# Performance work log

Hardware: AMD Instinct MI355X
Metric: run time of the kernel (lower is better)

The kernel has to match this reference:

```python
import jax, jax.numpy as jnp
import numpy as np
from jax import lax

B, C_IN, N, C_OUT, K = 16, 128, 2048, 256, 20
EPS = 1e-5


def setup_inputs() -> dict:
    key = jax.random.key(0)
    k1, k2 = jax.random.split(key)
    x = jax.random.normal(k1, (B, C_IN, N), dtype=jnp.float32)
    W = jax.random.normal(k2, (C_OUT, 2 * C_IN), dtype=jnp.float32) * (1.0 / np.sqrt(2 * C_IN))
    gamma = jnp.ones((C_OUT,), dtype=jnp.float32)
    beta = jnp.zeros((C_OUT,), dtype=jnp.float32)
    return {"x": x, "W": W, "gamma": gamma, "beta": beta, "k": K}


def _knn_inds(x, k):
    # squared pairwise distance: (B, N, N); computed with no grad (stop_gradient)
    xs = lax.stop_gradient(x)
    inner = jnp.einsum('bcn,bcm->bnm', xs, xs)
    sq = jnp.sum(xs * xs, axis=1)  # (B, N)
    pd = sq[:, :, None] - 2.0 * inner + sq[:, None, :]
    _, inds = lax.top_k(-pd, k)  # smallest distances -> (B, N, k)
    return inds


def reference(x, W, gamma, beta, k):
    knn = _knn_inds(x, k)                                   # (B, N, k) int
    # gather neighbours: neigh[b,c,n,j] = x[b,c,knn[b,n,j]]
    neigh = jax.vmap(lambda xb, kb: xb[:, kb])(x, knn)      # (B, C, N, k)
    central = jnp.broadcast_to(x[:, :, :, None], neigh.shape)
    edge = jnp.concatenate([central, neigh - central], axis=1)  # (B, 2C, N, k)
    # 1x1 conv (bias-free) as GEMM
    y = jnp.einsum('oc,bcnk->bonk', W, edge)                # (B, C_out, N, k)
    # BatchNorm2d (training-mode batch stats) + affine
    mean = jnp.mean(y, axis=(0, 2, 3), keepdims=True)
    var = jnp.var(y, axis=(0, 2, 3), keepdims=True)
    y = (y - mean) * lax.rsqrt(var + EPS)
    y = y * gamma[None, :, None, None] + beta[None, :, None, None]
    y = jax.nn.relu(y)
    return jnp.max(y, axis=3)                               # (B, C_out, N)
```

## Files before the change

### kernel.cpp

```cpp
#include <hip/hip_runtime.h>

#define B_   16
#define CIN  128
#define NPT  2048
#define COUT 256
#define KNN  20
#define KEEP 16
#define CAND 64
#define SIFT 32
#define EPS  1e-5f
#define DBIAS 256.0f

#define SQ_OFF   0ull
#define IDX_OFF  131072ull
#define UT_OFF   2752512ull
#define VT_OFF   36306944ull
#define GS_OFF   69861376ull
#define ST_OFF   69865472ull
#define AMAX_OFF 69871616ull
#define AMIN_OFF 103426048ull
#define WS_NEED_FUSED 136980480ull
#define XT_OFF   UT_OFF
#define XHT_OFF  VT_OFF

typedef _Float16 f16x8 __attribute__((ext_vector_type(8)));
typedef float    f32x4 __attribute__((ext_vector_type(4)));
typedef float    f32x2 __attribute__((ext_vector_type(2)));

__global__ __launch_bounds__(256) void prep_kernel(const float* __restrict__ x,
                                                   float* __restrict__ xT,
                                                   _Float16* __restrict__ xhT,
                                                   float* __restrict__ sqh) {
    __shared__ float Ls[128 * 68];
    __shared__ float ps[4 * 64];
    const int b = blockIdx.y, n0 = blockIdx.x * 64, t = threadIdx.x;
    const float* xb = x + (size_t)b * CIN * NPT;
    #pragma unroll
    for (int e = 0; e < 8; ++e) {
        int f = e * 256 + t;
        int c = f >> 4, n4 = (f & 15) << 2;
        *(float4*)&Ls[c * 68 + n4] = *(const float4*)&xb[(size_t)c * NPT + n0 + n4];
    }
    __syncthreads();
    {
        int nl = t & 63, part = t >> 6;
        float acc = 0.f;
        #pragma unroll
        for (int j = 0; j < 32; ++j) {
            float vh = (float)(_Float16)Ls[(part * 32 + j) * 68 + nl];
            acc += vh * vh;
        }
        ps[part * 64 + nl] = acc;
    }
    #pragma unroll
    for (int e = 0; e < 2; ++e) {
        int u = e * 256 + t;
        int nl = u >> 3, ck = (u & 7) << 4;
        float vv[16];
        #pragma unroll
        for (int j = 0; j < 16; ++j) vv[j] = Ls[(ck + j) * 68 + nl];
        size_t row = (size_t)b * NPT + n0 + nl;
        #pragma unroll
        for (int j = 0; j < 4; ++j) {
            float4 w = {vv[4 * j], vv[4 * j + 1], vv[4 * j + 2], vv[4 * j + 3]};
            *(float4*)&xT[row * CIN + ck + 4 * j] = w;
        }
        f16x8 h0, h1;
        #pragma unroll
        for (int j = 0; j < 8; ++j) { h0[j] = (_Float16)vv[j]; h1[j] = (_Float16)vv[8 + j]; }
        *(f16x8*)&xhT[row * CIN + ck] = h0;
        *(f16x8*)&xhT[row * CIN + ck + 8] = h1;
    }
    __syncthreads();
    if (t < 64) sqh[b * NPT + n0 + t] = ps[t] + ps[64 + t] + ps[128 + t] + ps[192 + t];
}

__global__ void wconv_kernel(const float* __restrict__ W,
                             _Float16* __restrict__ Wu,
                             _Float16* __restrict__ Wv) {
    int gid = blockIdx.x * 256 + threadIdx.x;
    int o = gid >> 7, c = gid & 127;
    float w1 = W[o * 256 + c], w2 = W[o * 256 + 128 + c];
    Wu[gid] = (_Float16)(w1 - w2);
    Wv[gid] = (_Float16)w2;
}

__device__ __forceinline__ void stage_pts(const _Float16* __restrict__ xhb,
                                          _Float16* buf, int base_n, int t) {
    const int l15 = t & 15, ks = t >> 6;
    const int quad = (t >> 4) & 3;
    const int c = ks * 32 + quad * 8;
    #pragma unroll
    for (int e = 0; e < 4; ++e) {
        const int n = base_n + e * 16 + l15;
        const _Float16* src = xhb + (size_t)n * CIN + c;
        _Float16* dst = buf + (size_t)(e * 256 + (t & 192)) * 8;
        __builtin_amdgcn_global_load_lds(
            (const __attribute__((address_space(1))) void*)src,
            (__attribute__((address_space(3))) void*)dst, 16, 0, 0);
    }
}

__device__ __forceinline__ void stage_tile16(const _Float16* __restrict__ srcl,
                                             _Float16* dsthalf) {
    #pragma unroll
    for (int e = 0; e < 4; ++e) {
        __builtin_amdgcn_global_load_lds(
            (const __attribute__((address_space(1))) void*)(srcl + e * 32),
            (__attribute__((address_space(3))) void*)(dsthalf + (size_t)e * 512),
            16, 0, 0);
    }
}

__global__ __launch_bounds__(256, 2) void knn_kernel(const _Float16* __restrict__ xhT,
                                                     const float* __restrict__ xT,
                                                     const float* __restrict__ sqh,
                                                     int* __restrict__ knn_out) {
    __shared__ char smraw[59392];
    _Float16* bufA = (_Float16*)smraw;
    float*    sqm  = (float*)(smraw + 18432);

    const int b  = blockIdx.y;
    const int q0 = blockIdx.x * 64;
    const int t  = threadIdx.x;
    const int lane = t & 63, wv = t >> 6;
    const int l15 = lane & 15, quad = lane >> 4;
    const _Float16* xhb = xhT + (size_t)b * NPT * CIN;

    #pragma unroll
    for (int e = 0; e < 8; ++e)
        sqm[e * 256 + t] = sqh[b * NPT + e * 256 + t] + DBIAS;

    stage_pts(xhb, bufA, q0, t);
    __syncthreads();

    f16x8 af[4][4];
    #pragma unroll
    for (int qh = 0; qh < 4; ++qh)
        #pragma unroll
        for (int ks = 0; ks < 4; ++ks)
            af[qh][ks] = *(const f16x8*)(bufA + (size_t)((qh * 4 + ks) * 64 + lane) * 8);
    __syncthreads();

    _Float16* wbuf = (_Float16*)(smraw + 26624 + wv * 8192);
    float*    DtW  = (float*)(smraw + wv * 4608);
    const _Float16* srcl = xhb + (size_t)(wv * 16 + l15) * CIN + quad * 8;

    stage_tile16(srcl, wbuf);

    float bd[KEEP];
    #pragma unroll
    for (int i = 0; i < KEEP; ++i) bd[i] = 3.0e38f;

    #pragma unroll 1
    for (int ss = 0; ss < 32; ++ss) {
        const int mb = ss * 64 + wv * 16;
        asm volatile("s_waitcnt vmcnt(0)" ::: "memory");
        __builtin_amdgcn_sched_barrier(0);
        const _Float16* cur = wbuf + (ss & 1) * 2048;
        f16x8 bf[4];
        #pragma unroll
        for (int ks = 0; ks < 4; ++ks)
            bf[ks] = *(const f16x8*)(cur + ks * 512 + quad * 128 + l15 * 8);
        float sm_ = sqm[mb + l15];
        asm volatile("s_waitcnt lgkmcnt(0)" ::: "memory");
        __builtin_amdgcn_sched_barrier(0);
        if (ss < 31)
            stage_tile16(srcl + (size_t)(ss + 1) * 64 * CIN,
                         wbuf + ((ss + 1) & 1) * 2048);
        __builtin_amdgcn_sched_barrier(0);
        f32x4 acc[4];
        #pragma unroll
        for (int qh = 0; qh < 4; ++qh) acc[qh] = (f32x4){0.f, 0.f, 0.f, 0.f};
        #pragma unroll
        for (int ks = 0; ks < 4; ++ks)
            #pragma unroll
            for (int qh = 0; qh < 4; ++qh)
                acc[qh] = __builtin_amdgcn_mfma_f32_16x16x32_f16(af[qh][ks], bf[ks], acc[qh], 0, 0, 0);
        const unsigned om = (unsigned)(mb + l15);
        #pragma unroll
        for (int qh = 0; qh < 4; ++qh) {
            #pragma unroll
            for (int rg = 0; rg < 4; ++rg) {
                int q = qh * 16 + quad * 4 + rg;
                float d = sm_ - 2.f * acc[qh][rg];
                DtW[q * 18 + l15] = __uint_as_float((__float_as_uint(d) & 0xFFFFF800u) | om);
            }
        }
        float nk[16];
        {
            const float* myrow = DtW + lane * 18;
            #pragma unroll
            for (int p = 0; p < 8; ++p) {
                f32x2 v = *(const f32x2*)(myrow + 2 * p);
                nk[2 * p] = v[0]; nk[2 * p + 1] = v[1];
            }
        }
        #pragma unroll
        for (int kk = 2; kk <= 16; kk <<= 1) {
            #pragma unroll
            for (int j = kk >> 1; j > 0; j >>= 1) {
                #pragma unroll
                for (int i = 0; i < 16; ++i) {
                    int p = i ^ j;
                    if (p > i) {
                        float a = nk[i], c = nk[p];
                        float lo = fminf(a, c), hi = fmaxf(a, c);
                        if ((i & kk) == 0) { nk[i] = lo; nk[p] = hi; }
                        else               { nk[i] = hi; nk[p] = lo; }
                    }
                }
            }
        }
        #pragma unroll
        for (int i = 0; i < 16; ++i) bd[i] = fminf(bd[i], nk[15 - i]);
        #pragma unroll
        for (int j = 8; j > 0; j >>= 1) {
            #pragma unroll
            for (int i = 0; i < 16; ++i) {
                int p = i ^ j;
                if (p > i) {
                    float a = bd[i], c = bd[p];
                    bd[i] = fminf(a, c);
                    bd[p] = fmaxf(a, c);
                }
            }
        }
    }

    __syncthreads();

    float*  Keys = (float*)smraw;
    int*    Surv = (int*)(smraw + 16640);
    double* ddL  = (double*)(smraw + 25088);
    #pragma unroll
    for (int i = 0; i < KEEP; ++i)
        Keys[lane * 65 + wv * KEEP + i] = bd[i];
    __syncthreads();
    {
        int cnt[KEEP];
        #pragma unroll
        for (int i = 0; i < KEEP; ++i) cnt[i] = 0;
        #pragma unroll 4
        for (int j = 0; j < CAND; ++j) {
            float kj = Keys[lane * 65 + j];
            #pragma unroll
            for (int i = 0; i < KEEP; ++i)
                cnt[i] += (kj < bd[i]) ? 1 : 0;
        }
        __syncthreads();
        #pragma unroll
        for (int i = 0; i < KEEP; ++i)
            if (cnt[i] < SIFT)
                Surv[lane * 33 + cnt[i]] = (int)(__float_as_uint(bd[i]) & 0x7FFu);
    }
    __syncthreads();

    int ms[8];
    #pragma unroll
    for (int k = 0; k < 8; ++k) ms[k] = Surv[lane * 33 + wv * 8 + k] & 2047;
    double dd8[8];
    #pragma unroll
    for (int k = 0; k < 8; ++k) dd8[k] = 0.0;
    const float* xTb = xT + (size_t)b * NPT * CIN;
    const float* qrow = xTb + (size_t)(q0 + lane) * CIN;
    #pragma unroll 1
    for (int ch = 0; ch < 8; ++ch) {
        double qd[16];
        #pragma unroll
        for (int j = 0; j < 4; ++j) {
            float4 qv = *(const float4*)&qrow[ch * 16 + 4 * j];
            qd[4 * j] = (double)qv.x; qd[4 * j + 1] = (double)qv.y;
            qd[4 * j + 2] = (double)qv.z; qd[4 * j + 3] = (double)qv.w;
        }
        #pragma unroll
        for (int k = 0; k < 8; ++k) {
            const float* mrow = xTb + (size_t)ms[k] * CIN + ch * 16;
            float4 ma = *(const float4*)&mrow[0];
            float4 mb2 = *(const float4*)&mrow[4];
            float4 mc = *(const float4*)&mrow[8];
            float4 md = *(const float4*)&mrow[12];
            double ss = dd8[k], d0;
            d0 = qd[0]  - (double)ma.x;  ss = fma(d0, d0, ss);
            d0 = qd[1]  - (double)ma.y;  ss = fma(d0, d0, ss);
            d0 = qd[2]  - (double)ma.z;  ss = fma(d0, d0, ss);
            d0 = qd[3]  - (double)ma.w;  ss = fma(d0, d0, ss);
            d0 = qd[4]  - (double)mb2.x; ss = fma(d0, d0, ss);
            d0 = qd[5]  - (double)mb2.y; ss = fma(d0, d0, ss);
            d0 = qd[6]  - (double)mb2.z; ss = fma(d0, d0, ss);
            d0 = qd[7]  - (double)mb2.w; ss = fma(d0, d0, ss);
            d0 = qd[8]  - (double)mc.x;  ss = fma(d0, d0, ss);
            d0 = qd[9]  - (double)mc.y;  ss = fma(d0, d0, ss);
            d0 = qd[10] - (double)mc.z;  ss = fma(d0, d0, ss);
            d0 = qd[11] - (double)mc.w;  ss = fma(d0, d0, ss);
            d0 = qd[12] - (double)md.x;  ss = fma(d0, d0, ss);
            d0 = qd[13] - (double)md.y;  ss = fma(d0, d0, ss);
            d0 = qd[14] - (double)md.z;  ss = fma(d0, d0, ss);
            d0 = qd[15] - (double)md.w;  ss = fma(d0, d0, ss);
            dd8[k] = ss;
        }
    }

    #pragma unroll
    for (int k = 0; k < 8; ++k) ddL[lane * 33 + wv * 8 + k] = dd8[k];
    __syncthreads();
    int* dst = knn_out + ((size_t)b * NPT + q0 + lane) * KNN;
    #pragma unroll
    for (int k = 0; k < 8; ++k) {
        int c = 0;
        #pragma unroll 4
        for (int j = 0; j < SIFT; ++j)
            c += (ddL[lane * 33 + j] < dd8[k]) ? 1 : 0;
        if (c < KNN) dst[c] = ms[k];
    }
}

__global__ __launch_bounds__(256) void uv_gemm_h(const _Float16* __restrict__ xhT,
                                                 const _Float16* __restrict__ Wu,
                                                 const _Float16* __restrict__ Wv,
                                                 float* __restrict__ uT,
                                                 float* __restrict__ vT) {
    __shared__ _Float16 Bx[8192];
    const int b = blockIdx.y, n0 = blockIdx.x * 64, t = threadIdx.x;
    const int lane = t & 63, w = t >> 6, l15 = lane & 15, quad = lane >> 4;
    stage_pts(xhT + (size_t)b * NPT * CIN, Bx, n0, t);
    __syncthreads();
    f16x8 bf[4];
    #pragma unroll
    for (int ks = 0; ks < 4; ++ks)
        bf[ks] = *(const f16x8*)(Bx + (size_t)((w * 4 + ks) * 64 + lane) * 8);
    const int n = n0 + w * 16 + l15;
    #pragma unroll 1
    for (int ot = 0; ot < 16; ++ot) {
        const _Float16* wu = Wu + (size_t)(ot * 16 + l15) * 128 + quad * 8;
        const _Float16* wv2 = Wv + (size_t)(ot * 16 + l15) * 128 + quad * 8;
        f32x4 au = (f32x4){0.f, 0.f, 0.f, 0.f};
        f32x4 av = (f32x4){0.f, 0.f, 0.f, 0.f};
        #pragma unroll
        for (int ks = 0; ks < 4; ++ks) {
            f16x8 a_u = *(const f16x8*)(wu + ks * 32);
            f16x8 a_v = *(const f16x8*)(wv2 + ks * 32);
            au = __builtin_amdgcn_mfma_f32_16x16x32_f16(a_u, bf[ks], au, 0, 0, 0);
            av = __builtin_amdgcn_mfma_f32_16x16x32_f16(a_v, bf[ks], av, 0, 0, 0);
        }
        size_t base = ((size_t)b * NPT + n) * COUT + ot * 16 + quad * 4;
        *(f32x4*)&uT[base] = au;
        *(f32x4*)&vT[base] = av;
    }
}

__global__ __launch_bounds__(256) void uv_gemm(const float* __restrict__ x,
                                               const float* __restrict__ W,
                                               float* __restrict__ uT,
                                               float* __restrict__ vT) {
    __shared__ float Ax[32 * 64];
    __shared__ float Bu[32 * 68];
    __shared__ float Bv[32 * 68];
    const int b  = blockIdx.z;
    const int n0 = blockIdx.x * 64;
    const int o0 = blockIdx.y * 64;
    const int t  = threadIdx.x;
    const int tx = t & 15, ty = t >> 4;
    const float* xb = x + (size_t)b * CIN * NPT;
    float au[4][4], av_[4][4];
    #pragma unroll
    for (int i = 0; i < 4; ++i)
        #pragma unroll
        for (int j = 0; j < 4; ++j) { au[i][j] = 0.f; av_[i][j] = 0.f; }
    #pragma unroll 1
    for (int kc = 0; kc < 4; ++kc) {
        const int c0 = kc * 32;
        __syncthreads();
        #pragma unroll
        for (int e = 0; e < 2; ++e) {
            int f = e * 256 + t;
            int cz = f >> 4, ni = (f & 15) << 2;
            *(float4*)&Ax[(cz << 6) + ni] = *(const float4*)&xb[(size_t)(c0 + cz) * NPT + n0 + ni];
        }
        #pragma unroll
        for (int e = 0; e < 8; ++e) {
            int ii = e * 256 + t;
            int cz = ii & 31, oj = ii >> 5;
            float w1 = W[(size_t)(o0 + oj) * 256 + c0 + cz];
            float w2 = W[(size_t)(o0 + oj) * 256 + 128 + c0 + cz];
            Bu[cz * 68 + oj] = w1 - w2;
            Bv[cz * 68 + oj] = w2;
        }
        __syncthreads();
        #pragma unroll 8
        for (int cz = 0; cz < 32; ++cz) {
            const float4 a4 = *(const float4*)&Ax[(cz << 6) + (tx << 2)];
            float bu0 = Bu[cz * 68 + (ty << 2) + 0], bv0 = Bv[cz * 68 + (ty << 2) + 0];
            float bu1 = Bu[cz * 68 + (ty << 2) + 1], bv1 = Bv[cz * 68 + (ty << 2) + 1];
            float bu2 = Bu[cz * 68 + (ty << 2) + 2], bv2 = Bv[cz * 68 + (ty << 2) + 2];
            float bu3 = Bu[cz * 68 + (ty << 2) + 3], bv3 = Bv[cz * 68 + (ty << 2) + 3];
            au[0][0] += a4.x * bu0; au[0][1] += a4.x * bu1; au[0][2] += a4.x * bu2; au[0][3] += a4.x * bu3;
            au[1][0] += a4.y * bu0; au[1][1] += a4.y * bu1; au[1][2] += a4.y * bu2; au[1][3] += a4.y * bu3;
            au[2][0] += a4.z * bu0; au[2][1] += a4.z * bu1; au[2][2] += a4.z * bu2; au[2][3] += a4.z * bu3;
            au[3][0] += a4.w * bu0; au[3][1] += a4.w * bu1; au[3][2] += a4.w * bu2; au[3][3] += a4.w * bu3;
            av_[0][0] += a4.x * bv0; av_[0][1] += a4.x * bv1; av_[0][2] += a4.x * bv2; av_[0][3] += a4.x * bv3;
            av_[1][0] += a4.y * bv0; av_[1][1] += a4.y * bv1; av_[1][2] += a4.y * bv2; av_[1][3] += a4.y * bv3;
            av_[2][0] += a4.z * bv0; av_[2][1] += a4.z * bv1; av_[2][2] += a4.z * bv2; av_[2][3] += a4.z * bv3;
            av_[3][0] += a4.w * bv0; av_[3][1] += a4.w * bv1; av_[3][2] += a4.w * bv2; av_[3][3] += a4.w * bv3;
        }
    }
    #pragma unroll
    for (int i = 0; i < 4; ++i) {
        int n = n0 + (tx << 2) + i;
        size_t base = ((size_t)b * NPT + n) * COUT + o0 + (ty << 2);
        float4 u4 = {au[i][0], au[i][1], au[i][2], au[i][3]};
        float4 v4 = {av_[i][0], av_[i][1], av_[i][2], av_[i][3]};
        *(float4*)&uT[base] = u4;
        *(float4*)&vT[base] = v4;
    }
}

__global__ __launch_bounds__(256) void gather_stats(const float* __restrict__ uT,
                                                    const float* __restrict__ vT,
                                                    const int* __restrict__ knn_in,
                                                    double* __restrict__ gsum,
                                                    float* __restrict__ aMax,
                                                    float* __restrict__ aMin) {
    __shared__ int sidx[16 * KNN];
    const int b  = blockIdx.y;
    const int n0 = blockIdx.x * 64 + blockIdx.z * 16;
    const int o  = threadIdx.x;
    for (int e = o; e < 16 * KNN; e += 256)
        sidx[e] = knn_in[((size_t)b * NPT + n0) * KNN + e];
    __syncthreads();
    const float* ub = uT + ((size_t)b * NPT + n0) * COUT + o;
    const float* vb = vT + (size_t)b * NPT * COUT + o;
    float* amx = aMax + ((size_t)b * NPT + n0) * COUT + o;
    float* amn = aMin + ((size_t)b * NPT + n0) * COUT + o;
    double s1 = 0.0, s2 = 0.0;
    #pragma unroll 1
    for (int s = 0; s < 16; ++s) {
        float u = ub[(size_t)s * COUT];
        float vmax = -3e38f, vmin = 3e38f, vsum = 0.f, vsq = 0.f;
        #pragma unroll
        for (int j = 0; j < KNN; ++j) {
            float v = vb[(size_t)sidx[s * KNN + j] * COUT];
            vmax = fmaxf(vmax, v);
            vmin = fminf(vmin, v);
            vsum += v;
            vsq = fmaf(v, v, vsq);
        }
        s1 += 20.0 * (double)u + (double)vsum;
        s2 += 20.0 * (double)u * (double)u + 2.0 * (double)u * (double)vsum + (double)vsq;
        amx[(size_t)s * COUT] = vmax;
        amn[(size_t)s * COUT] = vmin;
    }
    atomicAdd(&gsum[o], s1);
    atomicAdd(&gsum[COUT + o], s2);
}

__global__ __launch_bounds__(256) void stats_kernel(const float* __restrict__ uT,
                                                    const float* __restrict__ vT,
                                                    const int* __restrict__ knn_in,
                                                    double* __restrict__ gsum) {
    __shared__ int sidx[64 * KNN];
    const int b  = blockIdx.y;
    const int n0 = blockIdx.x * 64;
    const int o  = threadIdx.x;
    for (int e = o; e < 64 * KNN; e += 256)
        sidx[e] = knn_in[((size_t)b * NPT + n0) * KNN + e];
    __syncthreads();
    const float* ub = uT + ((size_t)b * NPT + n0) * COUT + o;
    const float* vb = vT + (size_t)b * NPT * COUT + o;
    double s1 = 0.0, s2 = 0.0;
    #pragma unroll 1
    for (int s = 0; s < 64; ++s) {
        float u = ub[(size_t)s * COUT];
        #pragma unroll
        for (int j = 0; j < KNN; ++j) {
            float y = u + vb[(size_t)sidx[s * KNN + j] * COUT];
            s1 += (double)y;
            s2 = fma((double)y, (double)y, s2);
        }
    }
    atomicAdd(&gsum[o], s1);
    atomicAdd(&gsum[COUT + o], s2);
}

__global__ void finalize_kernel(const double* __restrict__ gsum,
                                const float* __restrict__ gamma,
                                const float* __restrict__ beta,
                                float* __restrict__ st) {
    const int o = threadIdx.x;
    const double M = (double)B_ * NPT * KNN;
    double mean = gsum[o] / M;
    double var  = gsum[COUT + o] / M - mean * mean;
    float inv = 1.0f / sqrtf((float)var + EPS);
    float s = gamma[o] * inv;
    st[o] = s;
    st[COUT + o] = beta[o] - (float)mean * s;
}

__global__ __launch_bounds__(256, 2) void out2_kernel(const float* __restrict__ uT,
                                                      const float* __restrict__ aMax,
                                                      const float* __restrict__ aMin,
                                                      const float* __restrict__ st,
                                                      float* __restrict__ out) {
    __shared__ float zt[256 * 68];
    const int b  = blockIdx.y;
    const int n0 = blockIdx.x * 64;
    const int o  = threadIdx.x;
    const float s  = st[o];
    const float tt = st[COUT + o];
    const float* ub  = uT   + ((size_t)b * NPT + n0) * COUT + o;
    const float* amx = aMax + ((size_t)b * NPT + n0) * COUT + o;
    const float* amn = aMin + ((size_t)b * NPT + n0) * COUT + o;
    #pragma unroll 2
    for (int si = 0; si < 64; ++si) {
        float u = ub[(size_t)si * COUT];
        float y1 = u + amx[(size_t)si * COUT];
        float y2 = u + amn[(size_t)si * COUT];
        float z1 = fmaxf(s * y1 + tt, 0.f);
        float z2 = fmaxf(s * y2 + tt, 0.f);
        zt[o * 68 + si] = fmaxf(z1, z2);
    }
    __syncthreads();
    float* dst = out + ((size_t)b * COUT + o) * NPT + n0;
    #pragma unroll
    for (int i = 0; i < 16; ++i)
        *(float4*)&dst[i * 4] = *(const float4*)&zt[o * 68 + i * 4];
}

__global__ __launch_bounds__(256, 2) void out_kernel(const float* __restrict__ uT,
                                                     const float* __restrict__ vT,
                                                     const int* __restrict__ knn_in,
                                                     const float* __restrict__ st,
                                                     float* __restrict__ out) {
    __shared__ int sidx[64 * KNN];
    __shared__ float zt[256 * 68];
    const int b  = blockIdx.y;
    const int n0 = blockIdx.x * 64;
    const int o  = threadIdx.x;
    for (int e = o; e < 64 * KNN; e += 256)
        sidx[e] = knn_in[((size_t)b * NPT + n0) * KNN + e];
    __syncthreads();
    const float s  = st[o];
    const float tt = st[COUT + o];
    const float* ub = uT + ((size_t)b * NPT + n0) * COUT + o;
    const float* vb = vT + (size_t)b * NPT * COUT + o;
    #pragma unroll 1
    for (int si = 0; si < 64; ++si) {
        float u = ub[(size_t)si * COUT];
        float ymax = -3e38f, ymin = 3e38f;
        #pragma unroll
        for (int j = 0; j < KNN; ++j) {
            float y = u + vb[(size_t)sidx[si * KNN + j] * COUT];
            ymax = fmaxf(ymax, y);
            ymin = fminf(ymin, y);
        }
        float z1 = fmaxf(s * ymax + tt, 0.f);
        float z2 = fmaxf(s * ymin + tt, 0.f);
        zt[o * 68 + si] = fmaxf(z1, z2);
    }
    __syncthreads();
    float* dst = out + ((size_t)b * COUT + o) * NPT + n0;
    #pragma unroll
    for (int i = 0; i < 16; ++i)
        *(float4*)&dst[i * 4] = *(const float4*)&zt[o * 68 + i * 4];
}

extern "C" void kernel_launch(void* const* d_in, const int* in_sizes, int n_in,
                              void* d_out, int out_size, void* d_ws, size_t ws_size,
                              hipStream_t stream) {
    const float* x     = (const float*)d_in[0];
    const float* W     = (const float*)d_in[1];
    const float* gamma = (const float*)d_in[2];
    const float* beta  = (const float*)d_in[3];
    float* out = (float*)d_out;
    char* ws = (char*)d_ws;
    float*     sqh  = (float*)(ws + SQ_OFF);
    int*       idx  = (int*)(ws + IDX_OFF);
    float*     uT   = (float*)(ws + UT_OFF);
    float*     vT   = (float*)(ws + VT_OFF);
    double*    gsum = (double*)(ws + GS_OFF);
    float*     st   = (float*)(ws + ST_OFF);
    float*     aMax = (float*)(ws + AMAX_OFF);
    float*     aMin = (float*)(ws + AMIN_OFF);
    const bool fused = (ws_size >= WS_NEED_FUSED);

    hipMemsetAsync(gsum, 0, 2 * COUT * sizeof(double), stream);
    if (fused) {
        float*    xT  = (float*)(ws + AMAX_OFF);
        _Float16* xhT = (_Float16*)(ws + AMAX_OFF + 16777216ull);
        _Float16* Wu  = (_Float16*)(ws + AMAX_OFF + 25165824ull);
        _Float16* Wv  = (_Float16*)(ws + AMAX_OFF + 25231360ull);
        prep_kernel<<<dim3(32, 16), 256, 0, stream>>>(x, xT, xhT, sqh);
        wconv_kernel<<<128, 256, 0, stream>>>(W, Wu, Wv);
        knn_kernel<<<dim3(32, 16), 256, 0, stream>>>(xhT, xT, sqh, idx);
        uv_gemm_h<<<dim3(32, 16), 256, 0, stream>>>(xhT, Wu, Wv, uT, vT);
        gather_stats<<<dim3(32, 16, 4), 256, 0, stream>>>(uT, vT, idx, gsum, aMax, aMin);
        finalize_kernel<<<1, 256, 0, stream>>>(gsum, gamma, beta, st);
        out2_kernel<<<dim3(32, 16), 256, 0, stream>>>(uT, aMax, aMin, st, out);
    } else {
        float*    xT  = (float*)(ws + XT_OFF);
        _Float16* xhT = (_Float16*)(ws + XHT_OFF);
        prep_kernel<<<dim3(32, 16), 256, 0, stream>>>(x, xT, xhT, sqh);
        knn_kernel<<<dim3(32, 16), 256, 0, stream>>>(xhT, xT, sqh, idx);
        uv_gemm<<<dim3(32, 4, 16), 256, 0, stream>>>(x, W, uT, vT);
        stats_kernel<<<dim3(32, 16), 256, 0, stream>>>(uT, vT, idx, gsum);
        finalize_kernel<<<1, 256, 0, stream>>>(gsum, gamma, beta, st);
        out_kernel<<<dim3(32, 16), 256, 0, stream>>>(uT, vT, idx, st, out);
    }
}
```

Before: 352.2 us.

## Split kNN wave work into 32-query by 16-candidate tiles

Each wave in the kNN kernel now covers 32 queries against a 16-candidate tile over 64 steps, instead of all 64 queries over 32 steps. Each query's 64-candidate pool is spread across four sub-lists. Per step a lane sorts 8 new distances instead of 16 and merges them into the upper half of its kept list. This roughly halves the A-fragment registers and the LDS scratch per wave, and the next tile's prefetch is now issued before the current tile's reads. In exchange there are twice as many loop iterations, each running a full 16-wide merge, so total sorting work and loop overhead may grow.

```diff
diff --git a/kernel.cpp b/kernel.cpp
--- a/kernel.cpp
+++ b/kernel.cpp
@@ -116,15 +116,17 @@
                                                      const float* __restrict__ xT,
                                                      const float* __restrict__ sqh,
                                                      int* __restrict__ knn_out) {
-    __shared__ char smraw[59392];
+    __shared__ char smraw[57344];
     _Float16* bufA = (_Float16*)smraw;
-    float*    sqm  = (float*)(smraw + 18432);
+    float*    sqm  = (float*)(smraw + 16384);
 
     const int b  = blockIdx.y;
     const int q0 = blockIdx.x * 64;
     const int t  = threadIdx.x;
     const int lane = t & 63, wv = t >> 6;
     const int l15 = lane & 15, quad = lane >> 4;
+    const int qh2 = wv & 1;
+    const int mh  = wv >> 1;
     const _Float16* xhb = xhT + (size_t)b * NPT * CIN;
 
     #pragma unroll
@@ -134,74 +136,74 @@
     stage_pts(xhb, bufA, q0, t);
     __syncthreads();
 
-    f16x8 af[4][4];
-    #pragma unroll
-    for (int qh = 0; qh < 4; ++qh)
-        #pragma unroll
-        for (int ks = 0; ks < 4; ++ks)
-            af[qh][ks] = *(const f16x8*)(bufA + (size_t)((qh * 4 + ks) * 64 + lane) * 8);
-    __syncthreads();
-
-    _Float16* wbuf = (_Float16*)(smraw + 26624 + wv * 8192);
-    float*    DtW  = (float*)(smraw + wv * 4608);
-    const _Float16* srcl = xhb + (size_t)(wv * 16 + l15) * CIN + quad * 8;
-
+    f16x8 af0[4], af1[4];
+    #pragma unroll
+    for (int ks = 0; ks < 4; ++ks) {
+        af0[ks] = *(const f16x8*)(bufA + (size_t)((qh2 * 2) * 2048 + ks * 512 + lane * 8));
+        af1[ks] = *(const f16x8*)(bufA + (size_t)((qh2 * 2 + 1) * 2048 + ks * 512 + lane * 8));
+    }
+
+    _Float16* wbuf = (_Float16*)(smraw + 24576 + wv * 8192);
+    const _Float16* srcl = xhb + (size_t)(mh * 16 + l15) * CIN + quad * 8;
     stage_tile16(srcl, wbuf);
 
+    __syncthreads();
+    float* DtW = (float*)(smraw + wv * 2304);
+
     float bd[KEEP];
     #pragma unroll
     for (int i = 0; i < KEEP; ++i) bd[i] = 3.0e38f;
 
     #pragma unroll 1
-    for (int ss = 0; ss < 32; ++ss) {
-        const int mb = ss * 64 + wv * 16;
+    for (int ss = 0; ss < 64; ++ss) {
+        const int mb = (ss * 2 + mh) << 4;
         asm volatile("s_waitcnt vmcnt(0)" ::: "memory");
         __builtin_amdgcn_sched_barrier(0);
-        const _Float16* cur = wbuf + (ss & 1) * 2048;
-        f16x8 bf[4];
-        #pragma unroll
-        for (int ks = 0; ks < 4; ++ks)
-            bf[ks] = *(const f16x8*)(cur + ks * 512 + quad * 128 + l15 * 8);
-        float sm_ = sqm[mb + l15];
-        asm volatile("s_waitcnt lgkmcnt(0)" ::: "memory");
-        __builtin_amdgcn_sched_barrier(0);
-        if (ss < 31)
-            stage_tile16(srcl + (size_t)(ss + 1) * 64 * CIN,
+        if (ss < 63)
+            stage_tile16(srcl + (size_t)(ss + 1) * 32 * CIN,
                          wbuf + ((ss + 1) & 1) * 2048);
         __builtin_amdgcn_sched_barrier(0);
-        f32x4 acc[4];
-        #pragma unroll
-        for (int qh = 0; qh < 4; ++qh) acc[qh] = (f32x4){0.f, 0.f, 0.f, 0.f};
-        #pragma unroll
-        for (int ks = 0; ks < 4; ++ks)
+        const _Float16* cur = wbuf + (ss & 1) * 2048;
+        f16x8 bf0 = *(const f16x8*)(cur + 0 * 512 + lane * 8);
+        f16x8 bf1 = *(const f16x8*)(cur + 1 * 512 + lane * 8);
+        f16x8 bf2 = *(const f16x8*)(cur + 2 * 512 + lane * 8);
+        f16x8 bf3 = *(const f16x8*)(cur + 3 * 512 + lane * 8);
+        float sm_ = sqm[mb + l15];
+        f32x4 acc0 = (f32x4){0.f, 0.f, 0.f, 0.f};
+        f32x4 acc1 = (f32x4){0.f, 0.f, 0.f, 0.f};
+        acc0 = __builtin_amdgcn_mfma_f32_16x16x32_f16(af0[0], bf0, acc0, 0, 0, 0);
+        acc1 = __builtin_amdgcn_mfma_f32_16x16x32_f16(af1[0], bf0, acc1, 0, 0, 0);
+        acc0 = __builtin_amdgcn_mfma_f32_16x16x32_f16(af0[1], bf1, acc0, 0, 0, 0);
+        acc1 = __builtin_amdgcn_mfma_f32_16x16x32_f16(af1[1], bf1, acc1, 0, 0, 0);
+        acc0 = __builtin_amdgcn_mfma_f32_16x16x32_f16(af0[2], bf2, acc0, 0, 0, 0);
+        acc1 = __builtin_amdgcn_mfma_f32_16x16x32_f16(af1[2], bf2, acc1, 0, 0, 0);
+        acc0 = __builtin_amdgcn_mfma_f32_16x16x32_f16(af0[3], bf3, acc0, 0, 0, 0);
+        acc1 = __builtin_amdgcn_mfma_f32_16x16x32_f16(af1[3], bf3, acc1, 0, 0, 0);
+        const unsigned om = (unsigned)(mb + l15);
+        #pragma unroll
+        for (int rg = 0; rg < 4; ++rg) {
+            float d0 = sm_ - 2.f * acc0[rg];
+            DtW[(quad * 4 + rg) * 18 + l15] =
+                __uint_as_float((__float_as_uint(d0) & 0xFFFFF800u) | om);
+            float d1 = sm_ - 2.f * acc1[rg];
+            DtW[(16 + quad * 4 + rg) * 18 + l15] =
+                __uint_as_float((__float_as_uint(d1) & 0xFFFFF800u) | om);
+        }
+        float nk[8];
+        {
+            const float* myrow = DtW + (lane & 31) * 18 + (lane >> 5) * 8;
             #pragma unroll
-            for (int qh = 0; qh < 4; ++qh)
-                acc[qh] = __builtin_amdgcn_mfma_f32_16x16x32_f16(af[qh][ks], bf[ks], acc[qh], 0, 0, 0);
-        const unsigned om = (unsigned)(mb + l15);
-        #pragma unroll
-        for (int qh = 0; qh < 4; ++qh) {
-            #pragma unroll
-            for (int rg = 0; rg < 4; ++rg) {
-                int q = qh * 16 + quad * 4 + rg;
-                float d = sm_ - 2.f * acc[qh][rg];
-                DtW[q * 18 + l15] = __uint_as_float((__float_as_uint(d) & 0xFFFFF800u) | om);
-            }
-        }
-        float nk[16];
-        {
-            const float* myrow = DtW + lane * 18;
-            #pragma unroll
-            for (int p = 0; p < 8; ++p) {
+            for (int p = 0; p < 4; ++p) {
                 f32x2 v = *(const f32x2*)(myrow + 2 * p);
                 nk[2 * p] = v[0]; nk[2 * p + 1] = v[1];
             }
         }
         #pragma unroll
-        for (int kk = 2; kk <= 16; kk <<= 1) {
+        for (int kk = 2; kk <= 8; kk <<= 1) {
             #pragma unroll
             for (int j = kk >> 1; j > 0; j >>= 1) {
                 #pragma unroll
-                for (int i = 0; i < 16; ++i) {
+                for (int i = 0; i < 8; ++i) {
                     int p = i ^ j;
                     if (p > i) {
                         float a = nk[i], c = nk[p];
@@ -213,7 +215,7 @@
             }
         }
         #pragma unroll
-        for (int i = 0; i < 16; ++i) bd[i] = fminf(bd[i], nk[15 - i]);
+        for (int i = 0; i < 8; ++i) bd[8 + i] = fminf(bd[8 + i], nk[7 - i]);
         #pragma unroll
         for (int j = 8; j > 0; j >>= 1) {
             #pragma unroll
@@ -233,9 +235,11 @@
     float*  Keys = (float*)smraw;
     int*    Surv = (int*)(smraw + 16640);
     double* ddL  = (double*)(smraw + 25088);
+    const int q   = qh2 * 32 + (lane & 31);
+    const int sub = mh * 2 + (lane >> 5);
     #pragma unroll
     for (int i = 0; i < KEEP; ++i)
-        Keys[lane * 65 + wv * KEEP + i] = bd[i];
+        Keys[q * 65 + sub * KEEP + i] = bd[i];
     __syncthreads();
     {
         int cnt[KEEP];
@@ -243,7 +247,7 @@
         for (int i = 0; i < KEEP; ++i) cnt[i] = 0;
         #pragma unroll 4
         for (int j = 0; j < CAND; ++j) {
-            float kj = Keys[lane * 65 + j];
+            float kj = Keys[q * 65 + j];
             #pragma unroll
             for (int i = 0; i < KEEP; ++i)
                 cnt[i] += (kj < bd[i]) ? 1 : 0;
@@ -252,18 +256,18 @@
         #pragma unroll
         for (int i = 0; i < KEEP; ++i)
             if (cnt[i] < SIFT)
-                Surv[lane * 33 + cnt[i]] = (int)(__float_as_uint(bd[i]) & 0x7FFu);
+                Surv[q * 33 + cnt[i]] = (int)(__float_as_uint(bd[i]) & 0x7FFu);
     }
     __syncthreads();
 
     int ms[8];
     #pragma unroll
-    for (int k = 0; k < 8; ++k) ms[k] = Surv[lane * 33 + wv * 8 + k] & 2047;
+    for (int k = 0; k < 8; ++k) ms[k] = Surv[q * 33 + sub * 8 + k] & 2047;
     double dd8[8];
     #pragma unroll
     for (int k = 0; k < 8; ++k) dd8[k] = 0.0;
     const float* xTb = xT + (size_t)b * NPT * CIN;
-    const float* qrow = xTb + (size_t)(q0 + lane) * CIN;
+    const float* qrow = xTb + (size_t)(q0 + q) * CIN;
     #pragma unroll 1
     for (int ch = 0; ch < 8; ++ch) {
         double qd[16];
@@ -302,15 +306,15 @@
     }
 
     #pragma unroll
-    for (int k = 0; k < 8; ++k) ddL[lane * 33 + wv * 8 + k] = dd8[k];
-    __syncthreads();
-    int* dst = knn_out + ((size_t)b * NPT + q0 + lane) * KNN;
+    for (int k = 0; k < 8; ++k) ddL[q * 33 + sub * 8 + k] = dd8[k];
+    __syncthreads();
+    int* dst = knn_out + ((size_t)b * NPT + q0 + q) * KNN;
     #pragma unroll
     for (int k = 0; k < 8; ++k) {
         int c = 0;
         #pragma unroll 4
         for (int j = 0; j < SIFT; ++j)
-            c += (ddL[lane * 33 + j] < dd8[k]) ? 1 : 0;
+            c += (ddL[q * 33 + j] < dd8[k]) ? 1 : 0;
         if (c < KNN) dst[c] = ms[k];
     }
 }
```

Measured after the change: 369.2 us. 4.8% more time.

## Split kNN exact refinement into separate high-occupancy refine kernel

Applied to the files above, without the earlier changes.

The fp16 MFMA kNN kernel now stops after its candidate merge and writes 32 surviving candidate indices per query to workspace. A new refine_kernel, launched over 16-query blocks, recomputes the exact fp64 distances for those candidates and ranks them to produce the final 20 neighbours. The goal is to move the serial fp64 refinement out of the low-occupancy MFMA kernel and spread it across many more blocks. The cost is an extra launch and a workspace round trip for the survivor list. The old fused version is kept as knn_kernel_fb for the smaller-workspace fallback path.

```diff
diff --git a/kernel.cpp b/kernel.cpp
--- a/kernel.cpp
+++ b/kernel.cpp
@@ -113,9 +113,8 @@
 }
 
 __global__ __launch_bounds__(256, 2) void knn_kernel(const _Float16* __restrict__ xhT,
-                                                     const float* __restrict__ xT,
                                                      const float* __restrict__ sqh,
-                                                     int* __restrict__ knn_out) {
+                                                     int* __restrict__ surv_out) {
     __shared__ char smraw[59392];
     _Float16* bufA = (_Float16*)smraw;
     float*    sqm  = (float*)(smraw + 18432);
@@ -161,7 +160,219 @@
         f16x8 bf[4];
         #pragma unroll
         for (int ks = 0; ks < 4; ++ks)
-            bf[ks] = *(const f16x8*)(cur + ks * 512 + quad * 128 + l15 * 8);
+            bf[ks] = *(const f16x8*)(cur + ks * 512 + lane * 8);
+        float sm_ = sqm[mb + l15];
+        asm volatile("s_waitcnt lgkmcnt(0)" ::: "memory");
+        __builtin_amdgcn_sched_barrier(0);
+        if (ss < 31)
+            stage_tile16(srcl + (size_t)(ss + 1) * 64 * CIN,
+                         wbuf + ((ss + 1) & 1) * 2048);
+        __builtin_amdgcn_sched_barrier(0);
+        f32x4 acc[4];
+        #pragma unroll
+        for (int qh = 0; qh < 4; ++qh) acc[qh] = (f32x4){0.f, 0.f, 0.f, 0.f};
+        #pragma unroll
+        for (int ks = 0; ks < 4; ++ks)
+            #pragma unroll
+            for (int qh = 0; qh < 4; ++qh)
+                acc[qh] = __builtin_amdgcn_mfma_f32_16x16x32_f16(af[qh][ks], bf[ks], acc[qh], 0, 0, 0);
+        const unsigned om = (unsigned)(mb + l15);
+        #pragma unroll
+        for (int qh = 0; qh < 4; ++qh) {
+            #pragma unroll
+            for (int rg = 0; rg < 4; ++rg) {
+                int q = qh * 16 + quad * 4 + rg;
+                float d = sm_ - 2.f * acc[qh][rg];
+                DtW[q * 18 + l15] = __uint_as_float((__float_as_uint(d) & 0xFFFFF800u) | om);
+            }
+        }
+        float nk[16];
+        {
+            const float* myrow = DtW + lane * 18;
+            #pragma unroll
+            for (int p = 0; p < 8; ++p) {
+                f32x2 v = *(const f32x2*)(myrow + 2 * p);
+                nk[2 * p] = v[0]; nk[2 * p + 1] = v[1];
+            }
+        }
+        #pragma unroll
+        for (int kk = 2; kk <= 16; kk <<= 1) {
+            #pragma unroll
+            for (int j = kk >> 1; j > 0; j >>= 1) {
+                #pragma unroll
+                for (int i = 0; i < 16; ++i) {
+                    int p = i ^ j;
+                    if (p > i) {
+                        float a = nk[i], c = nk[p];
+                        float lo = fminf(a, c), hi = fmaxf(a, c);
+                        if ((i & kk) == 0) { nk[i] = lo; nk[p] = hi; }
+                        else               { nk[i] = hi; nk[p] = lo; }
+                    }
+                }
+            }
+        }
+        #pragma unroll
+        for (int i = 0; i < 16; ++i) bd[i] = fminf(bd[i], nk[15 - i]);
+        #pragma unroll
+        for (int j = 8; j > 0; j >>= 1) {
+            #pragma unroll
+            for (int i = 0; i < 16; ++i) {
+                int p = i ^ j;
+                if (p > i) {
+                    float a = bd[i], c = bd[p];
+                    bd[i] = fminf(a, c);
+                    bd[p] = fmaxf(a, c);
+                }
+            }
+        }
+    }
+
+    __syncthreads();
+
+    float* Keys = (float*)smraw;
+    #pragma unroll
+    for (int i = 0; i < KEEP; ++i)
+        Keys[lane * 65 + wv * KEEP + i] = bd[i];
+    __syncthreads();
+    {
+        int cnt[KEEP];
+        #pragma unroll
+        for (int i = 0; i < KEEP; ++i) cnt[i] = 0;
+        #pragma unroll 4
+        for (int j = 0; j < CAND; ++j) {
+            float kj = Keys[lane * 65 + j];
+            #pragma unroll
+            for (int i = 0; i < KEEP; ++i)
+                cnt[i] += (kj < bd[i]) ? 1 : 0;
+        }
+        int* dst = surv_out + ((size_t)b * NPT + q0 + lane) * SIFT;
+        #pragma unroll
+        for (int i = 0; i < KEEP; ++i)
+            if (cnt[i] < SIFT)
+                dst[cnt[i]] = (int)(__float_as_uint(bd[i]) & 0x7FFu);
+    }
+}
+
+__global__ __launch_bounds__(256, 4) void refine_kernel(const float* __restrict__ xT,
+                                                        const int* __restrict__ surv,
+                                                        int* __restrict__ knn_out) {
+    __shared__ float  Qs[16 * 128];
+    __shared__ int    sidx[16 * 32];
+    __shared__ double ddL[16 * 32];
+    const int b = blockIdx.y, q0 = blockIdx.x * 16, t = threadIdx.x;
+    const float* xTb = xT + (size_t)b * NPT * CIN;
+    #pragma unroll
+    for (int e = 0; e < 2; ++e)
+        sidx[e * 256 + t] = surv[((size_t)b * NPT + q0) * SIFT + e * 256 + t];
+    #pragma unroll
+    for (int e = 0; e < 2; ++e) {
+        int f = e * 256 + t;
+        int row = f >> 5, c4 = (f & 31) << 2;
+        *(float4*)&Qs[row * 128 + c4] = *(const float4*)&xTb[(size_t)(q0 + row) * CIN + c4];
+    }
+    __syncthreads();
+    const int g = t >> 3, j = t & 7;
+    #pragma unroll 1
+    for (int it = 0; it < 16; ++it) {
+        int pair = it * 32 + g;
+        int q = pair >> 5, k = pair & 31;
+        int m = sidx[q * 32 + k];
+        const float* mrow = xTb + (size_t)m * CIN + j * 16;
+        const float* qrow = Qs + q * 128 + j * 16;
+        float4 a0 = *(const float4*)&mrow[0];
+        float4 a1 = *(const float4*)&mrow[4];
+        float4 a2 = *(const float4*)&mrow[8];
+        float4 a3 = *(const float4*)&mrow[12];
+        float4 c0 = *(const float4*)&qrow[0];
+        float4 c1 = *(const float4*)&qrow[4];
+        float4 c2 = *(const float4*)&qrow[8];
+        float4 c3 = *(const float4*)&qrow[12];
+        double ss = 0.0, d0;
+        d0 = (double)c0.x - (double)a0.x; ss = fma(d0, d0, ss);
+        d0 = (double)c0.y - (double)a0.y; ss = fma(d0, d0, ss);
+        d0 = (double)c0.z - (double)a0.z; ss = fma(d0, d0, ss);
+        d0 = (double)c0.w - (double)a0.w; ss = fma(d0, d0, ss);
+        d0 = (double)c1.x - (double)a1.x; ss = fma(d0, d0, ss);
+        d0 = (double)c1.y - (double)a1.y; ss = fma(d0, d0, ss);
+        d0 = (double)c1.z - (double)a1.z; ss = fma(d0, d0, ss);
+        d0 = (double)c1.w - (double)a1.w; ss = fma(d0, d0, ss);
+        d0 = (double)c2.x - (double)a2.x; ss = fma(d0, d0, ss);
+        d0 = (double)c2.y - (double)a2.y; ss = fma(d0, d0, ss);
+        d0 = (double)c2.z - (double)a2.z; ss = fma(d0, d0, ss);
+        d0 = (double)c2.w - (double)a2.w; ss = fma(d0, d0, ss);
+        d0 = (double)c3.x - (double)a3.x; ss = fma(d0, d0, ss);
+        d0 = (double)c3.y - (double)a3.y; ss = fma(d0, d0, ss);
+        d0 = (double)c3.z - (double)a3.z; ss = fma(d0, d0, ss);
+        d0 = (double)c3.w - (double)a3.w; ss = fma(d0, d0, ss);
+        ss += __shfl_xor(ss, 1, 8);
+        ss += __shfl_xor(ss, 2, 8);
+        ss += __shfl_xor(ss, 4, 8);
+        if (j == 0) ddL[q * 32 + k] = ss;
+    }
+    __syncthreads();
+    const int q = t >> 4, kk = (t & 15) << 1;
+    int* dst = knn_out + ((size_t)b * NPT + q0 + q) * KNN;
+    #pragma unroll
+    for (int e = 0; e < 2; ++e) {
+        int k = kk + e;
+        double mine = ddL[q * 32 + k];
+        int c = 0;
+        #pragma unroll 4
+        for (int jx = 0; jx < SIFT; ++jx)
+            c += (ddL[q * 32 + jx] < mine) ? 1 : 0;
+        if (c < KNN) dst[c] = sidx[q * 32 + k];
+    }
+}
+
+__global__ __launch_bounds__(256, 2) void knn_kernel_fb(const _Float16* __restrict__ xhT,
+                                                        const float* __restrict__ xT,
+                                                        const float* __restrict__ sqh,
+                                                        int* __restrict__ knn_out) {
+    __shared__ char smraw[59392];
+    _Float16* bufA = (_Float16*)smraw;
+    float*    sqm  = (float*)(smraw + 18432);
+
+    const int b  = blockIdx.y;
+    const int q0 = blockIdx.x * 64;
+    const int t  = threadIdx.x;
+    const int lane = t & 63, wv = t >> 6;
+    const int l15 = lane & 15, quad = lane >> 4;
+    const _Float16* xhb = xhT + (size_t)b * NPT * CIN;
+
+    #pragma unroll
+    for (int e = 0; e < 8; ++e)
+        sqm[e * 256 + t] = sqh[b * NPT + e * 256 + t] + DBIAS;
+
+    stage_pts(xhb, bufA, q0, t);
+    __syncthreads();
+
+    f16x8 af[4][4];
+    #pragma unroll
+    for (int qh = 0; qh < 4; ++qh)
+        #pragma unroll
+        for (int ks = 0; ks < 4; ++ks)
+            af[qh][ks] = *(const f16x8*)(bufA + (size_t)((qh * 4 + ks) * 64 + lane) * 8);
+    __syncthreads();
+
+    _Float16* wbuf = (_Float16*)(smraw + 26624 + wv * 8192);
+    float*    DtW  = (float*)(smraw + wv * 4608);
+    const _Float16* srcl = xhb + (size_t)(wv * 16 + l15) * CIN + quad * 8;
+    stage_tile16(srcl, wbuf);
+
+    float bd[KEEP];
+    #pragma unroll
+    for (int i = 0; i < KEEP; ++i) bd[i] = 3.0e38f;
+
+    #pragma unroll 1
+    for (int ss = 0; ss < 32; ++ss) {
+        const int mb = ss * 64 + wv * 16;
+        asm volatile("s_waitcnt vmcnt(0)" ::: "memory");
+        __builtin_amdgcn_sched_barrier(0);
+        const _Float16* cur = wbuf + (ss & 1) * 2048;
+        f16x8 bf[4];
+        #pragma unroll
+        for (int ks = 0; ks < 4; ++ks)
+            bf[ks] = *(const f16x8*)(cur + ks * 512 + lane * 8);
         float sm_ = sqm[mb + l15];
         asm volatile("s_waitcnt lgkmcnt(0)" ::: "memory");
         __builtin_amdgcn_sched_barrier(0);
@@ -300,7 +511,6 @@
             dd8[k] = ss;
         }
     }
-
     #pragma unroll
     for (int k = 0; k < 8; ++k) ddL[lane * 33 + wv * 8 + k] = dd8[k];
     __syncthreads();
@@ -589,9 +799,11 @@
         _Float16* xhT = (_Float16*)(ws + AMAX_OFF + 16777216ull);
         _Float16* Wu  = (_Float16*)(ws + AMAX_OFF + 25165824ull);
         _Float16* Wv  = (_Float16*)(ws + AMAX_OFF + 25231360ull);
+        int*      svG = (int*)(ws + UT_OFF);
         prep_kernel<<<dim3(32, 16), 256, 0, stream>>>(x, xT, xhT, sqh);
         wconv_kernel<<<128, 256, 0, stream>>>(W, Wu, Wv);
-        knn_kernel<<<dim3(32, 16), 256, 0, stream>>>(xhT, xT, sqh, idx);
+        knn_kernel<<<dim3(32, 16), 256, 0, stream>>>(xhT, sqh, svG);
+        refine_kernel<<<dim3(128, 16), 256, 0, stream>>>(xT, svG, idx);
         uv_gemm_h<<<dim3(32, 16), 256, 0, stream>>>(xhT, Wu, Wv, uT, vT);
         gather_stats<<<dim3(32, 16, 4), 256, 0, stream>>>(uT, vT, idx, gsum, aMax, aMin);
         finalize_kernel<<<1, 256, 0, stream>>>(gsum, gamma, beta, st);
@@ -600,7 +812,7 @@
         float*    xT  = (float*)(ws + XT_OFF);
         _Float16* xhT = (_Float16*)(ws + XHT_OFF);
         prep_kernel<<<dim3(32, 16), 256, 0, stream>>>(x, xT, xhT, sqh);
-        knn_kernel<<<dim3(32, 16), 256, 0, stream>>>(xhT, xT, sqh, idx);
+        knn_kernel_fb<<<dim3(32, 16), 256, 0, stream>>>(xhT, xT, sqh, idx);
         uv_gemm<<<dim3(32, 4, 16), 256, 0, stream>>>(x, W, uT, vT);
         stats_kernel<<<dim3(32, 16), 256, 0, stream>>>(uT, vT, idx, gsum);
         finalize_kernel<<<1, 256, 0, stream>>>(gsum, gamma, beta, st);
```

Measured after the change: 336.8 us. 4.4% less time.
